# Kernel tuning notes

Measured on AMD Instinct MI355X. Metric: run time of the kernel, lower is better.

The kernel has to match this reference:

```python
import jax, jax.numpy as jnp
import numpy as np

N_HEAD = 16
ROPE_BASE = 10000.0


def rope_cos_sin(T, head_dim, dtype):
    inv_freq = 1.0 / (ROPE_BASE ** (jnp.arange(0, head_dim, 2, dtype=jnp.float32) / head_dim))
    t = jnp.arange(T, dtype=jnp.float32)
    freqs = jnp.einsum('i,j->ij', t, inv_freq)          # [T, head_dim/2]
    emb = jnp.concatenate([freqs, freqs], axis=-1)       # [T, head_dim]
    return jnp.cos(emb).astype(dtype), jnp.sin(emb).astype(dtype)


def rotate_half(x):
    h = x.shape[-1] // 2
    return jnp.concatenate([-x[..., h:], x[..., :h]], axis=-1)


def setup_inputs() -> dict:
    key = jax.random.key(0)
    ks = jax.random.split(key, 5)
    B, T, C = 2, 1024, 2048
    s = 0.02
    return {
        'x': jax.random.normal(ks[0], (B, T, C), dtype=jnp.float32),
        'Wq': jax.random.normal(ks[1], (C, C), dtype=jnp.float32) * s,
        'Wk': jax.random.normal(ks[2], (C, C), dtype=jnp.float32) * s,
        'Wv': jax.random.normal(ks[3], (C, C), dtype=jnp.float32) * s,
        'Wo': jax.random.normal(ks[4], (C, C), dtype=jnp.float32) * s,
    }


def reference(x, Wq, Wk, Wv, Wo):
    B, T, C = x.shape
    H = N_HEAD
    D = C // H
    # torch Linear: y = x @ W.T  (W is [out, in])
    q = jnp.einsum('btc,oc->bto', x, Wq).reshape(B, T, H, D).transpose(0, 2, 1, 3)
    k = jnp.einsum('btc,oc->bto', x, Wk).reshape(B, T, H, D).transpose(0, 2, 1, 3)
    v = jnp.einsum('btc,oc->bto', x, Wv).reshape(B, T, H, D).transpose(0, 2, 1, 3)
    cos, sin = rope_cos_sin(T, D, x.dtype)               # [T, D]
    cos = cos[None, None]                                 # [1,1,T,D]
    sin = sin[None, None]
    q = q * cos + rotate_half(q) * sin
    k = k * cos + rotate_half(k) * sin
    scale = 1.0 / jnp.sqrt(jnp.asarray(D, dtype=x.dtype))
    att = jnp.einsum('bhqd,bhkd->bhqk', q, k) * scale    # [B,H,T,T]
    causal = jnp.tril(jnp.ones((T, T), dtype=bool))
    att = jnp.where(causal[None, None], att, jnp.finfo(x.dtype).min)
    att = jax.nn.softmax(att, axis=-1)
    y = jnp.einsum('bhqk,bhkd->bhqd', att, v)            # [B,H,T,D]
    y = y.transpose(0, 2, 1, 3).reshape(B, T, C)
    return jnp.einsum('btc,oc->bto', y, Wo)
```

## Files before the change

kernel.cpp:

```cpp
#include <hip/hip_runtime.h>
#include <stdint.h>

typedef unsigned short u16;
typedef __bf16 bf16x8 __attribute__((ext_vector_type(8)));
typedef float  f32x4  __attribute__((ext_vector_type(4)));

#define B_  2
#define T_  1024
#define C_  2048
#define H_  16
#define D_  128
#define NTENS 4194304

__device__ __forceinline__ u16 f2bf(float f) {
    union { float f; uint32_t u; } v; v.f = f;
    uint32_t r = (v.u + 0x7FFFu + ((v.u >> 16) & 1u)) >> 16;
    return (u16)r;
}
__device__ __forceinline__ float bf2f(u16 h) {
    union { uint32_t u; float f; } v; v.u = ((uint32_t)h) << 16;
    return v.f;
}

__global__ __launch_bounds__(256) void k_convert(
    const float* __restrict__ x, const float* __restrict__ wq,
    const float* __restrict__ wk, const float* __restrict__ wv,
    const float* __restrict__ wo, u16* __restrict__ dst)
{
    int z = blockIdx.z;
    const float* src = (z == 0) ? x : (z == 1) ? wq : (z == 2) ? wk : (z == 3) ? wv : wo;
    u16* d = dst + (size_t)z * NTENS;
    size_t i = ((size_t)blockIdx.x * 256 + threadIdx.x) * 4;
    float4 v = *(const float4*)(src + i);
    ushort4 o;
    o.x = f2bf(v.x); o.y = f2bf(v.y); o.z = f2bf(v.z); o.w = f2bf(v.w);
    *(ushort4*)(d + i) = o;
}

__global__ __launch_bounds__(256) void k_rope(
    u16* __restrict__ q, u16* __restrict__ k)
{
    int idx = blockIdx.x * 256 + threadIdx.x;
    int d = idx & 63;
    int h = (idx >> 6) & 15;
    int t = (idx >> 10) & 1023;
    int b = idx >> 20;
    size_t base = ((size_t)(b * T_ + t)) * C_ + h * D_ + d;
    float inv = expf(-(float)d * (9.210340371976184f / 64.0f));
    float th = (float)t * inv;
    float s, c;
    sincosf(th, &s, &c);
    const float sc = 0.08838834764831845f;
    float q0 = bf2f(q[base]), q1 = bf2f(q[base + 64]);
    q[base]      = f2bf((q0 * c - q1 * s) * sc);
    q[base + 64] = f2bf((q1 * c + q0 * s) * sc);
    float k0 = bf2f(k[base]), k1 = bf2f(k[base + 64]);
    k[base]      = f2bf(k0 * c - k1 * s);
    k[base + 64] = f2bf(k1 * c + k0 * s);
}

__global__ __launch_bounds__(256) void k_transpose_v(
    const u16* __restrict__ vb, u16* __restrict__ vt)
{
    __shared__ u16 L[64 * 136];
    int t0 = blockIdx.x << 6;
    int bh = blockIdx.y, b = bh >> 4, h = bh & 15;
    const u16* src = vb + (size_t)b * (T_ * C_) + h * D_;
    u16* dst = vt + (size_t)bh * (D_ * T_);
    int tid = threadIdx.x;
#pragma unroll
    for (int i = 0; i < 4; ++i) {
        int idx = (i << 8) + tid;
        int r = idx >> 4, s = idx & 15;
        *(uint4*)&L[r * 136 + (s << 3)] =
            *(const uint4*)&src[(size_t)(t0 + r) * C_ + (s << 3)];
    }
    __syncthreads();
#pragma unroll
    for (int i = 0; i < 8; ++i) {
        int idx = (i << 8) + tid;
        int d = idx >> 4, s = idx & 15;
        int t = s << 2;
        ushort4 o;
        o.x = L[(t    ) * 136 + d];
        o.y = L[(t + 1) * 136 + d];
        o.z = L[(t + 2) * 136 + d];
        o.w = L[(t + 3) * 136 + d];
        *(ushort4*)&dst[(size_t)d * T_ + t0 + t] = o;
    }
}

template<typename OutT>
__device__ __forceinline__ void gemm_tile_nt(
    const u16* __restrict__ A, int lda,
    const u16* __restrict__ Bp, int ldb,
    OutT* __restrict__ Cp, int ldc,
    int m0, int n0, int K, float scale,
    u16* As, u16* Bs)
{
    const int tid  = threadIdx.x;
    const int wave = tid >> 6;
    const int lane = tid & 63;
    const int wr   = (wave >> 1) << 6;
    const int wc   = (wave & 1)  << 6;
    const int frow = lane & 15;
    const int quad = lane >> 4;

    const int lrow8  = lane >> 3;
    const int slot   = lane & 7;
    const int gchunk = slot ^ lrow8;

    f32x4 acc[4][4] = {};

    size_t aoff[4], boff[4];
#pragma unroll
    for (int i = 0; i < 4; ++i) {
        int r = (i << 5) + (wave << 3) + lrow8;
        aoff[i] = (size_t)(m0 + r) * lda + (gchunk << 3);
        boff[i] = (size_t)(n0 + r) * ldb + (gchunk << 3);
    }

    for (int kt = 0; kt < K; kt += 64) {
#pragma unroll
        for (int i = 0; i < 4; ++i) {
            int c = (i << 2) + wave;
            __builtin_amdgcn_global_load_lds(
                (const __attribute__((address_space(1))) void*)(A + aoff[i] + kt),
                (__attribute__((address_space(3))) void*)(As + (c << 9)), 16, 0, 0);
            __builtin_amdgcn_global_load_lds(
                (const __attribute__((address_space(1))) void*)(Bp + boff[i] + kt),
                (__attribute__((address_space(3))) void*)(Bs + (c << 9)), 16, 0, 0);
        }
        __syncthreads();

#pragma unroll
        for (int ks = 0; ks < 2; ++ks) {
            bf16x8 af[4], bfv[4];
#pragma unroll
            for (int i = 0; i < 4; ++i) {
                int ar = wr + (i << 4) + frow;
                int lk = (ks << 2) + quad;
                af[i] = *(const bf16x8*)&As[ar * 64 + ((lk ^ (frow & 7)) << 3)];
            }
#pragma unroll
            for (int j = 0; j < 4; ++j) {
                int br = wc + (j << 4) + frow;
                int lk = (ks << 2) + quad;
                bfv[j] = *(const bf16x8*)&Bs[br * 64 + ((lk ^ (frow & 7)) << 3)];
            }
#pragma unroll
            for (int i = 0; i < 4; ++i)
#pragma unroll
                for (int j = 0; j < 4; ++j)
                    acc[i][j] = __builtin_amdgcn_mfma_f32_16x16x32_bf16(
                        af[i], bfv[j], acc[i][j], 0, 0, 0);
        }
        __syncthreads();
    }

#pragma unroll
    for (int i = 0; i < 4; ++i)
#pragma unroll
        for (int j = 0; j < 4; ++j)
#pragma unroll
            for (int r = 0; r < 4; ++r) {
                int m = m0 + wr + (i << 4) + (quad << 2) + r;
                int n = n0 + wc + (j << 4) + frow;
                float val = acc[i][j][r] * scale;
                if constexpr (sizeof(OutT) == 2)
                    Cp[(size_t)m * ldc + n] = f2bf(val);
                else
                    Cp[(size_t)m * ldc + n] = val;
            }
}

__global__ __launch_bounds__(256) void k_gemm_qkv(
    const u16* __restrict__ xb, const u16* __restrict__ wq,
    const u16* __restrict__ wk, const u16* __restrict__ wv,
    u16* __restrict__ q, u16* __restrict__ k, u16* __restrict__ v)
{
    __shared__ u16 As[128 * 64], Bs[128 * 64];
    int z = blockIdx.z;
    const u16* Bp = (z == 0) ? wq : (z == 1) ? wk : wv;
    u16* Op       = (z == 0) ? q  : (z == 1) ? k  : v;
    gemm_tile_nt<u16>(xb, C_, Bp, C_, Op, C_,
                      blockIdx.y * 128, blockIdx.x * 128, C_, 1.0f, As, Bs);
}

__global__ __launch_bounds__(256) void k_flash(
    const u16* __restrict__ qb, const u16* __restrict__ kb,
    const u16* __restrict__ vt, u16* __restrict__ yb)
{
    __shared__ u16 Qs[64 * 128];
    __shared__ u16 Ks[64 * 128];
    __shared__ u16 Vs[128 * 64];

    const int bx  = blockIdx.x;
    const int bh  = bx & 31, b = bh >> 4, h = bh & 15;
    const int qt  = 15 - (bx >> 5);
    const int tid = threadIdx.x, wave = tid >> 6, lane = tid & 63;
    const int frow = lane & 15, quad = lane >> 4;

    const u16* qbase = qb + (size_t)b * (T_ * C_) + h * D_;
    const u16* kbase = kb + (size_t)b * (T_ * C_) + h * D_;
    const u16* vbase = vt + (size_t)bh * (D_ * T_);
    const int q0 = qt << 6;

    {
        const int r4 = lane >> 4, s16 = lane & 15;
#pragma unroll
        for (int i = 0; i < 4; ++i) {
            int c = (i << 2) + wave;
            int row = (c << 2) + r4;
            int g = (s16 & 8) | ((s16 & 7) ^ (row & 7));
            __builtin_amdgcn_global_load_lds(
                (const __attribute__((address_space(1))) void*)(qbase + (size_t)(q0 + row) * C_ + (g << 3)),
                (__attribute__((address_space(3))) void*)(Qs + (c << 9)), 16, 0, 0);
        }
    }

    f32x4 Y[8] = {};
    float mrow[4], lrow[4];
#pragma unroll
    for (int r = 0; r < 4; ++r) { mrow[r] = -3e38f; lrow[r] = 0.f; }

    const int tok = q0 + wave * 16 + quad * 4;

    for (int kt = 0; kt <= qt; ++kt) {
        const int k0 = kt << 6;
        {
            const int r4 = lane >> 4, s16 = lane & 15;
            const int r8 = lane >> 3, s8 = lane & 7;
#pragma unroll
            for (int i = 0; i < 4; ++i) {
                int c = (i << 2) + wave;
                int row = (c << 2) + r4;
                int g = (s16 & 8) | ((s16 & 7) ^ (row & 7));
                __builtin_amdgcn_global_load_lds(
                    (const __attribute__((address_space(1))) void*)(kbase + (size_t)(k0 + row) * C_ + (g << 3)),
                    (__attribute__((address_space(3))) void*)(Ks + (c << 9)), 16, 0, 0);
                int vrow = (c << 3) + r8;
                int vg = s8 ^ (vrow & 7);
                __builtin_amdgcn_global_load_lds(
                    (const __attribute__((address_space(1))) void*)(vbase + (size_t)vrow * T_ + k0 + (vg << 3)),
                    (__attribute__((address_space(3))) void*)(Vs + (c << 9)), 16, 0, 0);
            }
        }
        __syncthreads();

        f32x4 S[4] = {};
#pragma unroll
        for (int ks = 0; ks < 4; ++ks) {
            int lk = (ks << 2) + quad;
            int sw = ((lk & 8) | ((lk & 7) ^ (frow & 7))) << 3;
            bf16x8 a = *(const bf16x8*)&Qs[(wave * 16 + frow) * 128 + sw];
#pragma unroll
            for (int jj = 0; jj < 4; ++jj) {
                bf16x8 bb = *(const bf16x8*)&Ks[((jj << 4) + frow) * 128 + sw];
                S[jj] = __builtin_amdgcn_mfma_f32_16x16x32_bf16(a, bb, S[jj], 0, 0, 0);
            }
        }

        if (kt == qt) {
#pragma unroll
            for (int jj = 0; jj < 4; ++jj) {
                int colg = k0 + (jj << 4) + frow;
#pragma unroll
                for (int r = 0; r < 4; ++r)
                    if (colg > tok + r) S[jj][r] = -1e30f;
            }
        }

        float al[4];
#pragma unroll
        for (int r = 0; r < 4; ++r) {
            float tm = fmaxf(fmaxf(S[0][r], S[1][r]), fmaxf(S[2][r], S[3][r]));
#pragma unroll
            for (int off = 8; off > 0; off >>= 1) tm = fmaxf(tm, __shfl_xor(tm, off));
            float mn = fmaxf(mrow[r], tm);
            al[r] = __expf(mrow[r] - mn);
            mrow[r] = mn;
            float rs = 0.f;
#pragma unroll
            for (int jj = 0; jj < 4; ++jj) {
                float e = __expf(S[jj][r] - mn);
                S[jj][r] = e;
                rs += e;
            }
#pragma unroll
            for (int off = 8; off > 0; off >>= 1) rs += __shfl_xor(rs, off);
            lrow[r] = lrow[r] * al[r] + rs;
        }
#pragma unroll
        for (int dj = 0; dj < 8; ++dj)
#pragma unroll
            for (int r = 0; r < 4; ++r) Y[dj][r] *= al[r];

        __syncthreads();

        u16* Ps = Ks;
#pragma unroll
        for (int jj = 0; jj < 4; ++jj)
#pragma unroll
            for (int r = 0; r < 4; ++r)
                Ps[(wave * 16 + quad * 4 + r) * 72 + (jj << 4) + frow] = f2bf(S[jj][r]);

#pragma unroll
        for (int ks = 0; ks < 2; ++ks) {
            bf16x8 pa = *(const bf16x8*)&Ps[(wave * 16 + frow) * 72 + (ks << 5) + (quad << 3)];
            int lk = (ks << 2) + quad;
#pragma unroll
            for (int dj = 0; dj < 8; ++dj) {
                bf16x8 vv = *(const bf16x8*)&Vs[((dj << 4) + frow) * 64 + ((lk ^ (frow & 7)) << 3)];
                Y[dj] = __builtin_amdgcn_mfma_f32_16x16x32_bf16(pa, vv, Y[dj], 0, 0, 0);
            }
        }
        __syncthreads();
    }

    u16* ybase = yb + (size_t)b * (T_ * C_) + h * D_;
#pragma unroll
    for (int r = 0; r < 4; ++r) {
        float inv = 1.0f / lrow[r];
#pragma unroll
        for (int dj = 0; dj < 8; ++dj)
            ybase[(size_t)(tok + r) * C_ + (dj << 4) + frow] = f2bf(Y[dj][r] * inv);
    }
}

__global__ __launch_bounds__(256) void k_gemm_out(
    const u16* __restrict__ yb, const u16* __restrict__ wo, float* __restrict__ out)
{
    __shared__ u16 As[128 * 64], Bs[128 * 64];
    gemm_tile_nt<float>(yb, C_, wo, C_, out, C_,
                        blockIdx.y * 128, blockIdx.x * 128, C_, 1.0f, As, Bs);
}

extern "C" void kernel_launch(void* const* d_in, const int* in_sizes, int n_in,
                              void* d_out, int out_size, void* d_ws, size_t ws_size,
                              hipStream_t stream)
{
    (void)in_sizes; (void)n_in; (void)out_size; (void)ws_size;
    const float* x  = (const float*)d_in[0];
    const float* Wq = (const float*)d_in[1];
    const float* Wk = (const float*)d_in[2];
    const float* Wv = (const float*)d_in[3];
    const float* Wo = (const float*)d_in[4];

    u16* ws  = (u16*)d_ws;
    u16* xb  = ws;
    u16* wqb = ws + (size_t)1 * NTENS;
    u16* wkb = ws + (size_t)2 * NTENS;
    u16* wvb = ws + (size_t)3 * NTENS;
    u16* wob = ws + (size_t)4 * NTENS;
    u16* qb  = ws + (size_t)5 * NTENS;
    u16* kb  = ws + (size_t)6 * NTENS;
    u16* vb  = ws + (size_t)7 * NTENS;
    u16* yb  = ws + (size_t)8 * NTENS;
    u16* vt  = ws + (size_t)9 * NTENS;

    k_convert    <<<dim3(4096, 1, 5), 256, 0, stream>>>(x, Wq, Wk, Wv, Wo, ws);
    k_gemm_qkv   <<<dim3(16, 16, 3), 256, 0, stream>>>(xb, wqb, wkb, wvb, qb, kb, vb);
    k_rope       <<<dim3(8192), 256, 0, stream>>>(qb, kb);
    k_transpose_v<<<dim3(16, 32), 256, 0, stream>>>(vb, vt);
    k_flash      <<<dim3(512), 256, 0, stream>>>(qb, kb, vt, yb);
    k_gemm_out   <<<dim3(16, 16, 1), 256, 0, stream>>>(yb, wob, (float*)d_out);
}
```

Baseline: 285.8 us.

## Halve GEMM M-tile, fold V transpose into flash, precompute RoPE table

Three separate changes. The shared GEMM tile goes from 128x128 to 64x128, with each wave now covering 64x32, which doubles the grid for the QKV and output projections to improve CU occupancy at the cost of more reloads of B and less reuse per block. The separate V-transpose kernel is removed, and the flash kernel now transposes V into padded LDS with scalar stores every iteration. RoPE cos/sin are precomputed into a table by a small kernel instead of calling sincosf per element.

```diff
diff --git a/kernel.cpp b/kernel.cpp
--- a/kernel.cpp
+++ b/kernel.cpp
@@ -37,8 +37,20 @@
     *(ushort4*)(d + i) = o;
 }
 
+__global__ void k_rope_table(float* __restrict__ ct, float* __restrict__ st)
+{
+    int t = blockIdx.x, d = threadIdx.x;
+    float inv = expf(-(float)d * (9.210340371976184f / 64.0f));
+    float th = (float)t * inv;
+    float s, c;
+    sincosf(th, &s, &c);
+    ct[t * 64 + d] = c;
+    st[t * 64 + d] = s;
+}
+
 __global__ __launch_bounds__(256) void k_rope(
-    u16* __restrict__ q, u16* __restrict__ k)
+    u16* __restrict__ q, u16* __restrict__ k,
+    const float* __restrict__ ct, const float* __restrict__ st)
 {
     int idx = blockIdx.x * 256 + threadIdx.x;
     int d = idx & 63;
@@ -46,10 +58,7 @@
     int t = (idx >> 10) & 1023;
     int b = idx >> 20;
     size_t base = ((size_t)(b * T_ + t)) * C_ + h * D_ + d;
-    float inv = expf(-(float)d * (9.210340371976184f / 64.0f));
-    float th = (float)t * inv;
-    float s, c;
-    sincosf(th, &s, &c);
+    float c = ct[t * 64 + d], s = st[t * 64 + d];
     const float sc = 0.08838834764831845f;
     float q0 = bf2f(q[base]), q1 = bf2f(q[base + 64]);
     q[base]      = f2bf((q0 * c - q1 * s) * sc);
@@ -59,37 +68,6 @@
     k[base + 64] = f2bf(k1 * c + k0 * s);
 }
 
-__global__ __launch_bounds__(256) void k_transpose_v(
-    const u16* __restrict__ vb, u16* __restrict__ vt)
-{
-    __shared__ u16 L[64 * 136];
-    int t0 = blockIdx.x << 6;
-    int bh = blockIdx.y, b = bh >> 4, h = bh & 15;
-    const u16* src = vb + (size_t)b * (T_ * C_) + h * D_;
-    u16* dst = vt + (size_t)bh * (D_ * T_);
-    int tid = threadIdx.x;
-#pragma unroll
-    for (int i = 0; i < 4; ++i) {
-        int idx = (i << 8) + tid;
-        int r = idx >> 4, s = idx & 15;
-        *(uint4*)&L[r * 136 + (s << 3)] =
-            *(const uint4*)&src[(size_t)(t0 + r) * C_ + (s << 3)];
-    }
-    __syncthreads();
-#pragma unroll
-    for (int i = 0; i < 8; ++i) {
-        int idx = (i << 8) + tid;
-        int d = idx >> 4, s = idx & 15;
-        int t = s << 2;
-        ushort4 o;
-        o.x = L[(t    ) * 136 + d];
-        o.y = L[(t + 1) * 136 + d];
-        o.z = L[(t + 2) * 136 + d];
-        o.w = L[(t + 3) * 136 + d];
-        *(ushort4*)&dst[(size_t)d * T_ + t0 + t] = o;
-    }
-}
-
 template<typename OutT>
 __device__ __forceinline__ void gemm_tile_nt(
     const u16* __restrict__ A, int lda,
@@ -101,8 +79,7 @@
     const int tid  = threadIdx.x;
     const int wave = tid >> 6;
     const int lane = tid & 63;
-    const int wr   = (wave >> 1) << 6;
-    const int wc   = (wave & 1)  << 6;
+    const int wc   = wave << 5;
     const int frow = lane & 15;
     const int quad = lane >> 4;
 
@@ -110,23 +87,31 @@
     const int slot   = lane & 7;
     const int gchunk = slot ^ lrow8;
 
-    f32x4 acc[4][4] = {};
-
-    size_t aoff[4], boff[4];
+    f32x4 acc[4][2] = {};
+
+    size_t aoff[2], boff[4];
+#pragma unroll
+    for (int i = 0; i < 2; ++i) {
+        int r = (i << 5) + (wave << 3) + lrow8;
+        aoff[i] = (size_t)(m0 + r) * lda + (gchunk << 3);
+    }
 #pragma unroll
     for (int i = 0; i < 4; ++i) {
         int r = (i << 5) + (wave << 3) + lrow8;
-        aoff[i] = (size_t)(m0 + r) * lda + (gchunk << 3);
         boff[i] = (size_t)(n0 + r) * ldb + (gchunk << 3);
     }
 
     for (int kt = 0; kt < K; kt += 64) {
 #pragma unroll
-        for (int i = 0; i < 4; ++i) {
+        for (int i = 0; i < 2; ++i) {
             int c = (i << 2) + wave;
             __builtin_amdgcn_global_load_lds(
                 (const __attribute__((address_space(1))) void*)(A + aoff[i] + kt),
                 (__attribute__((address_space(3))) void*)(As + (c << 9)), 16, 0, 0);
+        }
+#pragma unroll
+        for (int i = 0; i < 4; ++i) {
+            int c = (i << 2) + wave;
             __builtin_amdgcn_global_load_lds(
                 (const __attribute__((address_space(1))) void*)(Bp + boff[i] + kt),
                 (__attribute__((address_space(3))) void*)(Bs + (c << 9)), 16, 0, 0);
@@ -135,23 +120,22 @@
 
 #pragma unroll
         for (int ks = 0; ks < 2; ++ks) {
-            bf16x8 af[4], bfv[4];
+            int lk = (ks << 2) + quad;
+            bf16x8 af[4], bfv[2];
 #pragma unroll
             for (int i = 0; i < 4; ++i) {
-                int ar = wr + (i << 4) + frow;
-                int lk = (ks << 2) + quad;
+                int ar = (i << 4) + frow;
                 af[i] = *(const bf16x8*)&As[ar * 64 + ((lk ^ (frow & 7)) << 3)];
             }
 #pragma unroll
-            for (int j = 0; j < 4; ++j) {
+            for (int j = 0; j < 2; ++j) {
                 int br = wc + (j << 4) + frow;
-                int lk = (ks << 2) + quad;
                 bfv[j] = *(const bf16x8*)&Bs[br * 64 + ((lk ^ (frow & 7)) << 3)];
             }
 #pragma unroll
             for (int i = 0; i < 4; ++i)
 #pragma unroll
-                for (int j = 0; j < 4; ++j)
+                for (int j = 0; j < 2; ++j)
                     acc[i][j] = __builtin_amdgcn_mfma_f32_16x16x32_bf16(
                         af[i], bfv[j], acc[i][j], 0, 0, 0);
         }
@@ -161,10 +145,10 @@
 #pragma unroll
     for (int i = 0; i < 4; ++i)
 #pragma unroll
-        for (int j = 0; j < 4; ++j)
+        for (int j = 0; j < 2; ++j)
 #pragma unroll
             for (int r = 0; r < 4; ++r) {
-                int m = m0 + wr + (i << 4) + (quad << 2) + r;
+                int m = m0 + (i << 4) + (quad << 2) + r;
                 int n = n0 + wc + (j << 4) + frow;
                 float val = acc[i][j][r] * scale;
                 if constexpr (sizeof(OutT) == 2)
@@ -179,21 +163,21 @@
     const u16* __restrict__ wk, const u16* __restrict__ wv,
     u16* __restrict__ q, u16* __restrict__ k, u16* __restrict__ v)
 {
-    __shared__ u16 As[128 * 64], Bs[128 * 64];
+    __shared__ u16 As[64 * 64], Bs[128 * 64];
     int z = blockIdx.z;
     const u16* Bp = (z == 0) ? wq : (z == 1) ? wk : wv;
     u16* Op       = (z == 0) ? q  : (z == 1) ? k  : v;
     gemm_tile_nt<u16>(xb, C_, Bp, C_, Op, C_,
-                      blockIdx.y * 128, blockIdx.x * 128, C_, 1.0f, As, Bs);
+                      blockIdx.y * 64, blockIdx.x * 128, C_, 1.0f, As, Bs);
 }
 
 __global__ __launch_bounds__(256) void k_flash(
     const u16* __restrict__ qb, const u16* __restrict__ kb,
-    const u16* __restrict__ vt, u16* __restrict__ yb)
+    const u16* __restrict__ vb, u16* __restrict__ yb)
 {
     __shared__ u16 Qs[64 * 128];
     __shared__ u16 Ks[64 * 128];
-    __shared__ u16 Vs[128 * 64];
+    __shared__ u16 Vs[128 * 72];
 
     const int bx  = blockIdx.x;
     const int bh  = bx & 31, b = bh >> 4, h = bh & 15;
@@ -203,7 +187,7 @@
 
     const u16* qbase = qb + (size_t)b * (T_ * C_) + h * D_;
     const u16* kbase = kb + (size_t)b * (T_ * C_) + h * D_;
-    const u16* vbase = vt + (size_t)bh * (D_ * T_);
+    const u16* vbase = vb + (size_t)b * (T_ * C_) + h * D_;
     const int q0 = qt << 6;
 
     {
@@ -230,7 +214,6 @@
         const int k0 = kt << 6;
         {
             const int r4 = lane >> 4, s16 = lane & 15;
-            const int r8 = lane >> 3, s8 = lane & 7;
 #pragma unroll
             for (int i = 0; i < 4; ++i) {
                 int c = (i << 2) + wave;
@@ -239,11 +222,20 @@
                 __builtin_amdgcn_global_load_lds(
                     (const __attribute__((address_space(1))) void*)(kbase + (size_t)(k0 + row) * C_ + (g << 3)),
                     (__attribute__((address_space(3))) void*)(Ks + (c << 9)), 16, 0, 0);
-                int vrow = (c << 3) + r8;
-                int vg = s8 ^ (vrow & 7);
-                __builtin_amdgcn_global_load_lds(
-                    (const __attribute__((address_space(1))) void*)(vbase + (size_t)vrow * T_ + k0 + (vg << 3)),
-                    (__attribute__((address_space(3))) void*)(Vs + (c << 9)), 16, 0, 0);
+            }
+        }
+        {
+#pragma unroll
+            for (int i = 0; i < 4; ++i) {
+                int idx = (i << 8) + tid;
+                int kr = idx & 63;
+                int n8 = (idx >> 6) << 3;
+                uint4 vv = *(const uint4*)&vbase[(size_t)(k0 + kr) * C_ + n8];
+                u16 tmp[8];
+                *(uint4*)tmp = vv;
+#pragma unroll
+                for (int e = 0; e < 8; ++e)
+                    Vs[(n8 + e) * 72 + kr] = tmp[e];
             }
         }
         __syncthreads();
@@ -308,10 +300,9 @@
 #pragma unroll
         for (int ks = 0; ks < 2; ++ks) {
             bf16x8 pa = *(const bf16x8*)&Ps[(wave * 16 + frow) * 72 + (ks << 5) + (quad << 3)];
-            int lk = (ks << 2) + quad;
 #pragma unroll
             for (int dj = 0; dj < 8; ++dj) {
-                bf16x8 vv = *(const bf16x8*)&Vs[((dj << 4) + frow) * 64 + ((lk ^ (frow & 7)) << 3)];
+                bf16x8 vv = *(const bf16x8*)&Vs[((dj << 4) + frow) * 72 + (ks << 5) + (quad << 3)];
                 Y[dj] = __builtin_amdgcn_mfma_f32_16x16x32_bf16(pa, vv, Y[dj], 0, 0, 0);
             }
         }
@@ -331,9 +322,9 @@
 __global__ __launch_bounds__(256) void k_gemm_out(
     const u16* __restrict__ yb, const u16* __restrict__ wo, float* __restrict__ out)
 {
-    __shared__ u16 As[128 * 64], Bs[128 * 64];
+    __shared__ u16 As[64 * 64], Bs[128 * 64];
     gemm_tile_nt<float>(yb, C_, wo, C_, out, C_,
-                        blockIdx.y * 128, blockIdx.x * 128, C_, 1.0f, As, Bs);
+                        blockIdx.y * 64, blockIdx.x * 128, C_, 1.0f, As, Bs);
 }
 
 extern "C" void kernel_launch(void* const* d_in, const int* in_sizes, int n_in,
@@ -357,12 +348,13 @@
     u16* kb  = ws + (size_t)6 * NTENS;
     u16* vb  = ws + (size_t)7 * NTENS;
     u16* yb  = ws + (size_t)8 * NTENS;
-    u16* vt  = ws + (size_t)9 * NTENS;
-
-    k_convert    <<<dim3(4096, 1, 5), 256, 0, stream>>>(x, Wq, Wk, Wv, Wo, ws);
-    k_gemm_qkv   <<<dim3(16, 16, 3), 256, 0, stream>>>(xb, wqb, wkb, wvb, qb, kb, vb);
-    k_rope       <<<dim3(8192), 256, 0, stream>>>(qb, kb);
-    k_transpose_v<<<dim3(16, 32), 256, 0, stream>>>(vb, vt);
-    k_flash      <<<dim3(512), 256, 0, stream>>>(qb, kb, vt, yb);
-    k_gemm_out   <<<dim3(16, 16, 1), 256, 0, stream>>>(yb, wob, (float*)d_out);
-}
+    float* ct = (float*)(ws + (size_t)9 * NTENS);
+    float* st = ct + 65536;
+
+    k_convert   <<<dim3(4096, 1, 5), 256, 0, stream>>>(x, Wq, Wk, Wv, Wo, ws);
+    k_rope_table<<<dim3(1024), 64, 0, stream>>>(ct, st);
+    k_gemm_qkv  <<<dim3(16, 32, 3), 256, 0, stream>>>(xb, wqb, wkb, wvb, qb, kb, vb);
+    k_rope      <<<dim3(8192), 256, 0, stream>>>(qb, kb, ct, st);
+    k_flash     <<<dim3(512), 256, 0, stream>>>(qb, kb, vb, yb);
+    k_gemm_out  <<<dim3(16, 32, 1), 256, 0, stream>>>(yb, wob, (float*)d_out);
+}
```

Result: faster. 272.9 us (-4.5%).
